# Optimization experiments

Hardware: AMD Instinct MI355X
Metric: run time of the kernel (lower is better)

Reference implementation:

```python
import jax, jax.numpy as jnp
import numpy as np

VARIANCE = (0.1, 0.2)   # SSD variance from init_kwargs
TOP_K = 1000            # max detections / NMS candidates per (image, class)


def _pairwise_iou(b):
    # b: [K,4] in point form (x1,y1,x2,y2)
    area = jnp.maximum(b[:, 2] - b[:, 0], 0.0) * jnp.maximum(b[:, 3] - b[:, 1], 0.0)
    lt = jnp.maximum(b[:, None, :2], b[None, :, :2])
    rb = jnp.minimum(b[:, None, 2:], b[None, :, 2:])
    wh = jnp.maximum(rb - lt, 0.0)
    inter = wh[..., 0] * wh[..., 1]
    union = area[:, None] + area[None, :] - inter
    return inter / jnp.maximum(union, 1e-12)


def _nms_pack(points, csboxes, scores, conf_thresh, nms_thresh):
    # points/csboxes: [P,4]; scores: [P]. Returns [TOP_K, 5] = (score, cx, cy, w, h)
    K = TOP_K
    masked = jnp.where(scores >= conf_thresh, scores, -jnp.inf)
    vals, idx = jax.lax.top_k(masked, K)          # sorted descending
    p = points[idx]                                # [K,4] point form
    cs = csboxes[idx]                              # [K,4] center-size form
    valid = vals >= conf_thresh
    iou = _pairwise_iou(p)                         # [K,K]
    ar = jnp.arange(K)

    def body(i, keep):
        # box i (if kept) suppresses all lower-scored boxes with IoU > thresh
        sup = (iou[i] > nms_thresh) & (ar > i) & keep[i]
        return keep & ~sup

    keep = jax.lax.fori_loop(0, K, body, valid)
    rows = jnp.concatenate([vals[:, None], cs], axis=1)        # [K,5]
    pos = jnp.where(keep, jnp.cumsum(keep) - 1, K)             # compact kept rows to front
    out = jnp.zeros((K, 5), rows.dtype).at[pos].set(rows, mode='drop')
    return out


def setup_inputs() -> dict:
    key = jax.random.key(0)
    k1, k2, k3, k4 = jax.random.split(key, 4)
    B, P, C = 8, 120000, 5
    loc_data = jax.random.normal(k1, (B, 4, P), dtype=jnp.float32) * 0.5
    conf_data = jax.random.normal(k2, (B, C, P), dtype=jnp.float32)
    cxcy = jax.random.uniform(k3, (P, 2), dtype=jnp.float32)
    wh = 0.01 + 0.29 * jax.random.uniform(k4, (P, 2), dtype=jnp.float32)
    prior_data = jnp.concatenate([cxcy, wh], axis=1)           # (cx,cy,w,h) in [0,1]
    return {
        'loc_data': loc_data,
        'conf_data': conf_data,
        'prior_data': prior_data,
        'conf_thresh': jnp.float32(0.05),
        'nms_thresh': jnp.float32(0.5),
    }


def reference(loc_data, conf_data, prior_data, conf_thresh, nms_thresh):
    v0, v1 = VARIANCE
    # softmax over class dim, drop background class 0 -> [B, Cfg, P]
    conf = jax.nn.softmax(conf_data, axis=1)[:, 1:]
    loc = jnp.transpose(loc_data, (0, 2, 1))                   # [B,P,4]
    # SSD decode -> center-size boxes
    cxcy = prior_data[None, :, :2] + loc[..., :2] * v0 * prior_data[None, :, 2:]
    wh = prior_data[None, :, 2:] * jnp.exp(loc[..., 2:] * v1)
    cs = jnp.concatenate([cxcy, wh], axis=-1)                  # [B,P,4] center-size
    pts = jnp.concatenate([cxcy - wh / 2, cxcy + wh / 2], axis=-1)  # [B,P,4] point form
    per_class = jax.vmap(_nms_pack, in_axes=(None, None, 0, None, None))
    per_image = jax.vmap(per_class, in_axes=(0, 0, 0, None, None))
    return per_image(pts, cs, conf, conf_thresh, nms_thresh)   # [B, Cfg, TOP_K, 5]
```

## Files before the change

kernel.cpp:

```cpp
#include <hip/hip_runtime.h>
#include <cstdint>
#include <cstddef>

typedef unsigned long long ull;

#define KTOP   1000
#define CAP    4096
#define HBITS  14
#define HB     (1 << HBITS)
#define HSHIFT (32 - HBITS)
#define ROWS   1024
#define WORDS  16
#define HCHUNK 16

__global__ void decode_kernel(const float* __restrict__ loc,
                              const float* __restrict__ conf,
                              const float* __restrict__ prior,
                              float* __restrict__ scores,
                              float* __restrict__ cs,
                              unsigned* __restrict__ histz,
                              int histW,
                              int B, int C, int P) {
#pragma clang fp contract(off)
    int t = blockIdx.x * blockDim.x + threadIdx.x;

    for (int i = t; i < histW; i += gridDim.x * blockDim.x) histz[i] = 0u;

    if (t >= B * P) return;
    int b = t / P;
    int p = t - b * P;

    float x[8];
    float m = -INFINITY;
    for (int c = 0; c < C; ++c) {
        x[c] = conf[((size_t)b * C + c) * P + p];
        m = fmaxf(m, x[c]);
    }
    float sum = 0.f;
    for (int c = 0; c < C; ++c) {
        x[c] = expf(x[c] - m);
        sum += x[c];
    }
    for (int c = 1; c < C; ++c) {
        float v = x[c] / sum;
        int bc = b * (C - 1) + (c - 1);
        scores[(size_t)bc * P + p] = v;
    }

    float l0 = loc[((size_t)b * 4 + 0) * P + p];
    float l1 = loc[((size_t)b * 4 + 1) * P + p];
    float l2 = loc[((size_t)b * 4 + 2) * P + p];
    float l3 = loc[((size_t)b * 4 + 3) * P + p];
    float4 pr4 = *(const float4*)(prior + (size_t)p * 4);

    float cx = pr4.x + (l0 * 0.1f) * pr4.z;
    float cy = pr4.y + (l1 * 0.1f) * pr4.w;
    float w  = pr4.z * expf(l2 * 0.2f);
    float h  = pr4.w * expf(l3 * 0.2f);

    *(float4*)(cs + ((size_t)b * P + p) * 4) = make_float4(cx, cy, w, h);
}

__global__ void __launch_bounds__(256)
hist_kernel(const float* __restrict__ scores,
            const float* __restrict__ cthp,
            unsigned* __restrict__ hist,
            int P) {
    __shared__ unsigned sh[HB / 2];
    int bc  = blockIdx.x;
    int tid = threadIdx.x;
    float cth = *cthp;

    for (int i = tid; i < HB / 2; i += 256) sh[i] = 0u;
    __syncthreads();

    int chunk = (P + HCHUNK - 1) / HCHUNK;
    int lo = blockIdx.y * chunk;
    int hi = lo + chunk; if (hi > P) hi = P;
    const float* s = scores + (size_t)bc * P;
    for (int p = lo + tid; p < hi; p += 256) {
        float v = s[p];
        if (v >= cth) {
            unsigned bin = __float_as_uint(v) >> HSHIFT;
            atomicAdd(&sh[bin >> 1], (bin & 1u) ? 65536u : 1u);
        }
    }
    __syncthreads();

    unsigned* h = hist + (size_t)bc * HB;
    for (int i = tid; i < HB / 2; i += 256) {
        unsigned v = sh[i];
        if (v & 0xFFFFu)  atomicAdd(&h[2 * i],     v & 0xFFFFu);
        if (v >> 16)      atomicAdd(&h[2 * i + 1], v >> 16);
    }
}

__global__ void __launch_bounds__(256)
pivot_kernel(const unsigned* __restrict__ hist, unsigned* __restrict__ pivot) {
    int bc  = blockIdx.x;
    int t   = threadIdx.x;
    const unsigned* h = hist + (size_t)bc * HB;
    __shared__ unsigned T[256];

    const int per = HB / 256;
    int base = t * per;
    unsigned S = 0;
    for (int i = 0; i < per; ++i) S += h[base + i];
    T[t] = S;
    __syncthreads();

    for (int d = 1; d < 256; d <<= 1) {
        unsigned add = (t + d < 256) ? T[t + d] : 0u;
        __syncthreads();
        T[t] += add;
        __syncthreads();
    }

    unsigned Tt = T[t];
    unsigned Tn = (t + 1 < 256) ? T[t + 1] : 0u;
    if (Tt >= (unsigned)KTOP && Tn < (unsigned)KTOP) {
        unsigned cum = Tn;
        for (int i = per - 1; i >= 0; --i) {
            cum += h[base + i];
            if (cum >= (unsigned)KTOP) { pivot[bc] = (unsigned)(base + i); break; }
        }
    }
    if (t == 0 && T[0] < (unsigned)KTOP) pivot[bc] = 0u;
}

__global__ void __launch_bounds__(256)
gather_kernel(const float* __restrict__ scores,
              const unsigned* __restrict__ pivot,
              unsigned* __restrict__ cnt,
              ull* __restrict__ cand,
              const float* __restrict__ cthp, int P) {
    __shared__ unsigned wsum[4];
    __shared__ unsigned s_base;
    int bc = blockIdx.x;
    const float* s = scores + (size_t)bc * P;
    float cth = *cthp;
    unsigned pv = pivot[bc];
    int nchunk = gridDim.y;
    int chunk = (P + nchunk - 1) / nchunk;
    int lo = blockIdx.y * chunk;
    int hi = lo + chunk; if (hi > P) hi = P;
    int tid  = threadIdx.x;
    int lane = tid & 63;
    int wid  = tid >> 6;

    unsigned mycnt = 0;
    for (int p = lo + tid; p < hi; p += 256) {
        float v = s[p];
        unsigned k = __float_as_uint(v);
        if (v >= cth && (k >> HSHIFT) >= pv) ++mycnt;
    }
    unsigned x = mycnt;
    for (int d = 1; d < 64; d <<= 1) {
        unsigned y = (unsigned)__shfl_up((int)x, d);
        if (lane >= d) x += y;
    }
    if (lane == 63) wsum[wid] = x;
    __syncthreads();
    if (tid == 0) {
        unsigned tot = 0;
        for (int w = 0; w < 4; ++w) { unsigned t2 = wsum[w]; wsum[w] = tot; tot += t2; }
        s_base = tot ? atomicAdd(&cnt[bc], tot) : 0u;
    }
    __syncthreads();
    unsigned off = s_base + wsum[wid] + (x - mycnt);

    ull* cb = cand + (size_t)bc * CAP;
    for (int p = lo + tid; p < hi; p += 256) {
        float v = s[p];
        unsigned k = __float_as_uint(v);
        if (v >= cth && (k >> HSHIFT) >= pv) {
            if (off < CAP)
                cb[off] = ((ull)k << 32) | (unsigned)(~(unsigned)p);
            ++off;
        }
    }
}

__global__ void __launch_bounds__(1024)
sort_kernel(const ull* __restrict__ cand,
            const unsigned* __restrict__ cnt,
            const float* __restrict__ cs,
            float* __restrict__ rows,
            float4* __restrict__ pbox,
            float* __restrict__ bar,
            int* __restrict__ nselArr,
            int P, int Cfg) {
#pragma clang fp contract(off)
    int bc  = blockIdx.x;
    int b   = bc / Cfg;
    int tid = threadIdx.x;
    __shared__ ull sbuf[CAP];

    int M = (int)cnt[bc]; if (M > CAP) M = CAP;
    int nsel = M < KTOP ? M : KTOP;
    if (tid == 0) nselArr[bc] = nsel;

    int n = 1024;
    while (n < M) n <<= 1;
    for (int i = tid; i < n; i += 1024)
        sbuf[i] = (i < M) ? cand[(size_t)bc * CAP + i] : 0ull;
    __syncthreads();

    for (unsigned k = 2; k <= (unsigned)n; k <<= 1) {
        for (unsigned j = k >> 1; j > 0; j >>= 1) {
            for (unsigned i = tid; i < (unsigned)n; i += 1024) {
                unsigned ixj = i ^ j;
                if (ixj > i) {
                    bool up = ((i & k) == 0u);
                    ull a = sbuf[i], bb = sbuf[ixj];
                    if ((a > bb) == up) { sbuf[i] = bb; sbuf[ixj] = a; }
                }
            }
            __syncthreads();
        }
    }

    for (int r = tid; r < nsel; r += 1024) {
        ull e = sbuf[n - 1 - r];
        float sc = __uint_as_float((unsigned)(e >> 32));
        int idx = (int)(~(unsigned)e);
        const float* c4 = cs + ((size_t)b * P + idx) * 4;
        float cx = c4[0], cy = c4[1], w = c4[2], h = c4[3];
        float x1 = cx - w / 2.f, y1 = cy - h / 2.f;
        float x2 = cx + w / 2.f, y2 = cy + h / 2.f;
        size_t sb = (size_t)bc * ROWS + r;
        pbox[sb] = make_float4(x1, y1, x2, y2);
        bar[sb]  = fmaxf(x2 - x1, 0.f) * fmaxf(y2 - y1, 0.f);
        float* rr = rows + ((size_t)bc * KTOP + r) * 5;
        rr[0] = sc; rr[1] = cx; rr[2] = cy; rr[3] = w; rr[4] = h;
    }
}

__global__ void __launch_bounds__(1024)
mask_kernel(const float4* __restrict__ pbox,
            const float* __restrict__ bar,
            const int* __restrict__ nselArr,
            const float* __restrict__ nthp,
            ull* __restrict__ mask) {
#pragma clang fp contract(off)
    int bc   = blockIdx.x;
    int tile = blockIdx.y;
    int tid  = threadIdx.x;
    int nsel = nselArr[bc];
    float nth = *nthp;

    __shared__ float4 sbox[ROWS];
    __shared__ float  sar[ROWS];
    size_t sb = (size_t)bc * ROWS;
    sbox[tid] = pbox[sb + tid];
    sar[tid]  = bar[sb + tid];
    __syncthreads();

    int wv   = tid >> 6;
    int lane = tid & 63;
    int i0   = tile * 64 + (wv << 2);

    float4 bi[4]; float ai[4];
    #pragma unroll
    for (int r = 0; r < 4; ++r) { bi[r] = sbox[i0 + r]; ai[r] = sar[i0 + r]; }

    ull rowbits[4] = {0ull, 0ull, 0ull, 0ull};
    for (int w = 0; w < WORDS; ++w) {
        int j = (w << 6) + lane;
        float4 bj = sbox[j];
        float  aj = sar[j];
        #pragma unroll
        for (int r = 0; r < 4; ++r) {
            int i = i0 + r;
            float ww = fmaxf(fminf(bi[r].z, bj.z) - fmaxf(bi[r].x, bj.x), 0.f);
            float hh = fmaxf(fminf(bi[r].w, bj.w) - fmaxf(bi[r].y, bj.y), 0.f);
            float inter = ww * hh;
            float uni = ai[r] + aj - inter;
            float iou = inter / fmaxf(uni, 1e-12f);
            bool ok = (j > i) && (j < nsel) && (iou > nth);
            ull bits = __ballot(ok);
            if (lane == w) rowbits[r] = bits;
        }
    }
    #pragma unroll
    for (int r = 0; r < 4; ++r)
        if (lane < WORDS)
            mask[(((size_t)bc * ROWS + (i0 + r)) << 4) + lane] = rowbits[r];
}

__device__ __forceinline__ void nms_chunk_body(
    int c, int nchunk, int lane, int g, int w,
    const ull* __restrict__ mrow, ull* sm,
    ull (&pr)[16], ull (&st)[16], ull& S)
{
    int cb = (c & 1) << 10;
    int nb = ((c + 1) & 1) << 10;
    if (c + 2 < nchunk) {
        #pragma unroll
        for (int k = 0; k < 16; ++k)
            pr[k] = mrow[(size_t)(c + 2) * 1024 + k * 64 + lane];
    }

    ull cur = __shfl(S, c);
    ull dbuf[16], dnxt[16];
    #pragma unroll
    for (int k = 0; k < 16; ++k) dbuf[k] = sm[cb + (k << 4) + c];
    #pragma unroll
    for (int grp = 0; grp < 4; ++grp) {
        if (grp < 3) {
            #pragma unroll
            for (int k = 0; k < 16; ++k)
                dnxt[k] = sm[cb + ((((grp + 1) << 4) + k) << 4) + c];
        }
        #pragma unroll
        for (int k = 0; k < 16; ++k) {
            int i = (grp << 4) + k;
            ull supm = (ull)((long long)(cur << (63 - i)) >> 63);
            cur |= dbuf[k] & ~supm;
        }
        if (grp < 3) {
            #pragma unroll
            for (int k = 0; k < 16; ++k) dbuf[k] = dnxt[k];
        }
    }
    ull kbits = ~cur;

    unsigned sub = (unsigned)((kbits >> (g << 4)) & 0xFFFFull);
    int rbase2 = cb + (g << 8) + w;
    ull part = 0ull;
    #pragma unroll
    for (int i = 0; i < 16; ++i) {
        ull v = sm[rbase2 + (i << 4)];
        part |= v & (ull)(0ll - (long long)((sub >> i) & 1u));
    }
    part |= __shfl_xor(part, 16);
    part |= __shfl_xor(part, 32);
    S |= part;
    if (lane == c) S = cur;

    if (c + 1 < nchunk) {
        #pragma unroll
        for (int k = 0; k < 16; ++k) sm[nb + k * 64 + lane] = st[k];
    }
}

__global__ void __launch_bounds__(256)
reduce_pack_kernel(const ull* __restrict__ mask,
                   const int* __restrict__ nselArr,
                   const float* __restrict__ rows,
                   float* __restrict__ out) {
    int bc  = blockIdx.x;
    int tid = threadIdx.x;
    int nsel = nselArr[bc];
    const ull* mrow = mask + ((size_t)bc * ROWS << 4);

    __shared__ ull sm[2048];
    __shared__ ull kw[WORDS];
    __shared__ unsigned pref[WORDS + 1];

    if (tid < 64) {
        int lane = tid;
        int nchunk = (nsel + 63) >> 6;
        ull S = 0ull;
        int g = lane >> 4;
        int w = lane & 15;

        ull ra[16], rb[16];
        if (nchunk > 0) {
            #pragma unroll
            for (int k = 0; k < 16; ++k) ra[k] = mrow[k * 64 + lane];
            if (nchunk > 1) {
                #pragma unroll
                for (int k = 0; k < 16; ++k) rb[k] = mrow[1024 + k * 64 + lane];
            }
            #pragma unroll
            for (int k = 0; k < 16; ++k) sm[k * 64 + lane] = ra[k];

            #pragma unroll 1
            for (int cc = 0; cc < 8; ++cc) {
                int c0 = cc << 1;
                if (c0 >= nchunk) break;
                nms_chunk_body(c0, nchunk, lane, g, w, mrow, sm, ra, rb, S);
                int c1 = c0 + 1;
                if (c1 >= nchunk) break;
                nms_chunk_body(c1, nchunk, lane, g, w, mrow, sm, rb, ra, S);
            }
        }

        if (lane < WORDS) {
            int base_i = lane << 6;
            ull valid = 0ull;
            int rem = nsel - base_i;
            if (rem > 0) valid = (rem >= 64) ? ~0ull : ((1ull << rem) - 1ull);
            kw[lane] = (~S) & valid;
        }
    }
    __syncthreads();

    if (tid == 0) {
        unsigned c = 0;
        for (int w = 0; w < WORDS; ++w) { pref[w] = c; c += (unsigned)__popcll(kw[w]); }
        pref[WORDS] = c;
    }
    __syncthreads();
    unsigned tot = pref[WORDS];

    const float* rbase = rows + (size_t)bc * KTOP * 5;
    float* obase = out + (size_t)bc * KTOP * 5;
    for (int r = tid; r < KTOP; r += 256) {
        ull wv = kw[r >> 6];
        if ((wv >> (r & 63)) & 1ull) {
            int pos = (int)pref[r >> 6] + __popcll(wv & ((1ull << (r & 63)) - 1ull));
            const float* rr = rbase + r * 5;
            float* oo = obase + pos * 5;
            oo[0] = rr[0]; oo[1] = rr[1]; oo[2] = rr[2]; oo[3] = rr[3]; oo[4] = rr[4];
        }
        if (r >= (int)tot) {
            float* oo = obase + r * 5;
            oo[0] = 0.f; oo[1] = 0.f; oo[2] = 0.f; oo[3] = 0.f; oo[4] = 0.f;
        }
    }
}

extern "C" void kernel_launch(void* const* d_in, const int* in_sizes, int n_in,
                              void* d_out, int out_size, void* d_ws, size_t ws_size,
                              hipStream_t stream) {
    (void)n_in; (void)out_size; (void)ws_size;
    const float* loc   = (const float*)d_in[0];
    const float* conf  = (const float*)d_in[1];
    const float* prior = (const float*)d_in[2];
    const float* cth   = (const float*)d_in[3];
    const float* nth   = (const float*)d_in[4];
    float* out = (float*)d_out;

    int P   = in_sizes[2] / 4;
    int B   = in_sizes[0] / (4 * P);
    int C   = in_sizes[1] / (B * P);
    int Cfg = C - 1;
    int NBC = B * Cfg;

    char* base = (char*)d_ws;
    size_t off = 0;
    auto carve = [&](size_t bytes) { char* p = base + off; off = (off + bytes + 255) & ~(size_t)255; return p; };

    float4*   pbox   = (float4*)  carve((size_t)NBC * ROWS * 16);
    ull*      cand   = (ull*)     carve((size_t)NBC * CAP * 8);
    ull*      mask   = (ull*)     carve((size_t)NBC * ROWS * WORDS * 8);
    float*    scores = (float*)   carve((size_t)NBC * P * 4);
    float*    cs     = (float*)   carve((size_t)B * P * 4 * 4);
    float*    rows   = (float*)   carve((size_t)NBC * KTOP * 5 * 4);
    float*    bar    = (float*)   carve((size_t)NBC * ROWS * 4);
    unsigned* hist   = (unsigned*)carve((size_t)NBC * HB * 4 + (size_t)NBC * 4);
    unsigned* cnt    = hist + (size_t)NBC * HB;
    unsigned* pivot  = (unsigned*)carve((size_t)NBC * 4);
    int*      nselA  = (int*)     carve((size_t)NBC * 4);

    int histW = NBC * HB + NBC;

    int n1 = B * P;
    decode_kernel<<<(n1 + 255) / 256, 256, 0, stream>>>(loc, conf, prior, scores, cs, hist, histW, B, C, P);
    hist_kernel<<<dim3(NBC, HCHUNK), 256, 0, stream>>>(scores, cth, hist, P);
    pivot_kernel<<<NBC, 256, 0, stream>>>(hist, pivot);
    gather_kernel<<<dim3(NBC, 32), 256, 0, stream>>>(scores, pivot, cnt, cand, cth, P);
    sort_kernel<<<NBC, 1024, 0, stream>>>(cand, cnt, cs, rows, pbox, bar, nselA, P, Cfg);
    mask_kernel<<<dim3(NBC, ROWS / 64), 1024, 0, stream>>>(pbox, bar, nselA, nth, mask);
    reduce_pack_kernel<<<NBC, 256, 0, stream>>>(mask, nselA, rows, out);
}
```

Measured before the change: 210.6 us.

## Defer box decode to selected candidates, fuse pivot into hist, single-pass gather

Drops full box decoding from the decode kernel and decodes only the selected top candidates inside the sort kernel. The pivot kernel is folded into the histogram kernel using a last-block-done atomic counter. Gather becomes single-pass, staging through LDS with ballot compaction. Sort adds a secondary histogram pre-filter so it sorts about 1024 entries instead of up to 4096, and the mask kernel skips tiles and words below the diagonal or beyond nsel. Together these cut global memory traffic, kernel launches and sort work, at the cost of added atomics and more complex code.

```diff
diff --git a/kernel.cpp b/kernel.cpp
--- a/kernel.cpp
+++ b/kernel.cpp
@@ -12,12 +12,10 @@
 #define ROWS   1024
 #define WORDS  16
 #define HCHUNK 16
-
-__global__ void decode_kernel(const float* __restrict__ loc,
-                              const float* __restrict__ conf,
-                              const float* __restrict__ prior,
+#define GSTAGE 4096
+
+__global__ void decode_kernel(const float* __restrict__ conf,
                               float* __restrict__ scores,
-                              float* __restrict__ cs,
                               unsigned* __restrict__ histz,
                               int histW,
                               int B, int C, int P) {
@@ -46,27 +44,18 @@
         int bc = b * (C - 1) + (c - 1);
         scores[(size_t)bc * P + p] = v;
     }
-
-    float l0 = loc[((size_t)b * 4 + 0) * P + p];
-    float l1 = loc[((size_t)b * 4 + 1) * P + p];
-    float l2 = loc[((size_t)b * 4 + 2) * P + p];
-    float l3 = loc[((size_t)b * 4 + 3) * P + p];
-    float4 pr4 = *(const float4*)(prior + (size_t)p * 4);
-
-    float cx = pr4.x + (l0 * 0.1f) * pr4.z;
-    float cy = pr4.y + (l1 * 0.1f) * pr4.w;
-    float w  = pr4.z * expf(l2 * 0.2f);
-    float h  = pr4.w * expf(l3 * 0.2f);
-
-    *(float4*)(cs + ((size_t)b * P + p) * 4) = make_float4(cx, cy, w, h);
 }
 
 __global__ void __launch_bounds__(256)
 hist_kernel(const float* __restrict__ scores,
             const float* __restrict__ cthp,
             unsigned* __restrict__ hist,
+            unsigned* __restrict__ done,
+            unsigned* __restrict__ pivot,
             int P) {
     __shared__ unsigned sh[HB / 2];
+    __shared__ unsigned T[256];
+    __shared__ unsigned s_tk;
     int bc  = blockIdx.x;
     int tid = threadIdx.x;
     float cth = *cthp;
@@ -93,39 +82,40 @@
         if (v & 0xFFFFu)  atomicAdd(&h[2 * i],     v & 0xFFFFu);
         if (v >> 16)      atomicAdd(&h[2 * i + 1], v >> 16);
     }
-}
-
-__global__ void __launch_bounds__(256)
-pivot_kernel(const unsigned* __restrict__ hist, unsigned* __restrict__ pivot) {
-    int bc  = blockIdx.x;
-    int t   = threadIdx.x;
-    const unsigned* h = hist + (size_t)bc * HB;
-    __shared__ unsigned T[256];
+    __syncthreads();
+
+    if (tid == 0) {
+        __threadfence();
+        s_tk = __hip_atomic_fetch_add(&done[bc], 1u, __ATOMIC_ACQ_REL, __HIP_MEMORY_SCOPE_AGENT);
+    }
+    __syncthreads();
+    if (s_tk != (unsigned)(gridDim.y - 1)) return;
 
     const int per = HB / 256;
-    int base = t * per;
+    int base = tid * per;
     unsigned S = 0;
-    for (int i = 0; i < per; ++i) S += h[base + i];
-    T[t] = S;
+    for (int i = 0; i < per; ++i)
+        S += __hip_atomic_load(&h[base + i], __ATOMIC_RELAXED, __HIP_MEMORY_SCOPE_AGENT);
+    T[tid] = S;
     __syncthreads();
 
     for (int d = 1; d < 256; d <<= 1) {
-        unsigned add = (t + d < 256) ? T[t + d] : 0u;
-        __syncthreads();
-        T[t] += add;
-        __syncthreads();
-    }
-
-    unsigned Tt = T[t];
-    unsigned Tn = (t + 1 < 256) ? T[t + 1] : 0u;
+        unsigned add = (tid + d < 256) ? T[tid + d] : 0u;
+        __syncthreads();
+        T[tid] += add;
+        __syncthreads();
+    }
+
+    unsigned Tt = T[tid];
+    unsigned Tn = (tid + 1 < 256) ? T[tid + 1] : 0u;
     if (Tt >= (unsigned)KTOP && Tn < (unsigned)KTOP) {
         unsigned cum = Tn;
         for (int i = per - 1; i >= 0; --i) {
-            cum += h[base + i];
+            cum += __hip_atomic_load(&h[base + i], __ATOMIC_RELAXED, __HIP_MEMORY_SCOPE_AGENT);
             if (cum >= (unsigned)KTOP) { pivot[bc] = (unsigned)(base + i); break; }
         }
     }
-    if (t == 0 && T[0] < (unsigned)KTOP) pivot[bc] = 0u;
+    if (tid == 0 && T[0] < (unsigned)KTOP) pivot[bc] = 0u;
 }
 
 __global__ void __launch_bounds__(256)
@@ -134,7 +124,8 @@
               unsigned* __restrict__ cnt,
               ull* __restrict__ cand,
               const float* __restrict__ cthp, int P) {
-    __shared__ unsigned wsum[4];
+    __shared__ ull stage[GSTAGE];
+    __shared__ unsigned l_cnt;
     __shared__ unsigned s_base;
     int bc = blockIdx.x;
     const float* s = scores + (size_t)bc * P;
@@ -146,45 +137,48 @@
     int hi = lo + chunk; if (hi > P) hi = P;
     int tid  = threadIdx.x;
     int lane = tid & 63;
-    int wid  = tid >> 6;
-
-    unsigned mycnt = 0;
-    for (int p = lo + tid; p < hi; p += 256) {
-        float v = s[p];
-        unsigned k = __float_as_uint(v);
-        if (v >= cth && (k >> HSHIFT) >= pv) ++mycnt;
-    }
-    unsigned x = mycnt;
-    for (int d = 1; d < 64; d <<= 1) {
-        unsigned y = (unsigned)__shfl_up((int)x, d);
-        if (lane >= d) x += y;
-    }
-    if (lane == 63) wsum[wid] = x;
-    __syncthreads();
-    if (tid == 0) {
-        unsigned tot = 0;
-        for (int w = 0; w < 4; ++w) { unsigned t2 = wsum[w]; wsum[w] = tot; tot += t2; }
-        s_base = tot ? atomicAdd(&cnt[bc], tot) : 0u;
-    }
-    __syncthreads();
-    unsigned off = s_base + wsum[wid] + (x - mycnt);
-
+
+    if (tid == 0) l_cnt = 0u;
+    __syncthreads();
+
+    for (int p0 = lo; p0 < hi; p0 += 256) {
+        int p = p0 + tid;
+        bool q = false; unsigned k = 0u;
+        if (p < hi) {
+            float v = s[p];
+            k = __float_as_uint(v);
+            q = (v >= cth) && ((k >> HSHIFT) >= pv);
+        }
+        ull mb = __ballot(q);
+        if (mb) {
+            unsigned wbase = 0u;
+            if (lane == 0) wbase = atomicAdd(&l_cnt, (unsigned)__popcll(mb));
+            wbase = (unsigned)__shfl((int)wbase, 0);
+            if (q) {
+                unsigned pos = wbase + (unsigned)__popcll(mb & ((1ull << lane) - 1ull));
+                stage[pos] = ((ull)k << 32) | (unsigned)(~(unsigned)p);
+            }
+        }
+    }
+    __syncthreads();
+
+    unsigned tot = l_cnt;
+    if (tid == 0) s_base = tot ? atomicAdd(&cnt[bc], tot) : 0u;
+    __syncthreads();
+    unsigned base = s_base;
     ull* cb = cand + (size_t)bc * CAP;
-    for (int p = lo + tid; p < hi; p += 256) {
-        float v = s[p];
-        unsigned k = __float_as_uint(v);
-        if (v >= cth && (k >> HSHIFT) >= pv) {
-            if (off < CAP)
-                cb[off] = ((ull)k << 32) | (unsigned)(~(unsigned)p);
-            ++off;
-        }
+    for (unsigned i = tid; i < tot; i += 256) {
+        unsigned off = base + i;
+        if (off < CAP) cb[off] = stage[i];
     }
 }
 
 __global__ void __launch_bounds__(1024)
 sort_kernel(const ull* __restrict__ cand,
             const unsigned* __restrict__ cnt,
-            const float* __restrict__ cs,
+            const unsigned* __restrict__ pivot,
+            const float* __restrict__ loc,
+            const float* __restrict__ prior,
             float* __restrict__ rows,
             float4* __restrict__ pbox,
             float* __restrict__ bar,
@@ -195,15 +189,61 @@
     int b   = bc / Cfg;
     int tid = threadIdx.x;
     __shared__ ull sbuf[CAP];
+    __shared__ unsigned h2[1024];
+    __shared__ unsigned s_hi, s_spv, s_m2, s_pos;
 
     int M = (int)cnt[bc]; if (M > CAP) M = CAP;
     int nsel = M < KTOP ? M : KTOP;
     if (tid == 0) nselArr[bc] = nsel;
 
+    for (int i = tid; i < M; i += 1024)
+        sbuf[i] = cand[(size_t)bc * CAP + i];
+    __syncthreads();
+
+    int Meff = M;
+    if (M > 1024) {
+        unsigned pv = pivot[bc];
+        h2[tid] = 0u;
+        if (tid == 0) { s_hi = 0u; s_pos = 0u; s_spv = 0u; s_m2 = (unsigned)M; }
+        __syncthreads();
+        for (int i = tid; i < M; i += 1024) {
+            unsigned sb32 = (unsigned)(sbuf[i] >> 32);
+            if ((sb32 >> HSHIFT) > pv) atomicAdd(&s_hi, 1u);
+            else atomicAdd(&h2[(sb32 >> 8) & 1023u], 1u);
+        }
+        __syncthreads();
+        unsigned hicnt = s_hi;
+        for (int d = 1; d < 1024; d <<= 1) {
+            unsigned add = (tid + d < 1024) ? h2[tid + d] : 0u;
+            __syncthreads();
+            h2[tid] += add;
+            __syncthreads();
+        }
+        unsigned A  = hicnt + h2[tid];
+        unsigned Bv = hicnt + ((tid + 1 < 1024) ? h2[tid + 1] : 0u);
+        if (A >= (unsigned)KTOP && Bv < (unsigned)KTOP) { s_spv = (unsigned)tid; s_m2 = A; }
+        __syncthreads();
+        unsigned thr24 = ((unsigned)pv << 10) | s_spv;
+        Meff = (int)s_m2;
+        ull my[4];
+        #pragma unroll
+        for (int j = 0; j < 4; ++j) { int i = tid + (j << 10); my[j] = (i < M) ? sbuf[i] : 0ull; }
+        __syncthreads();
+        #pragma unroll
+        for (int j = 0; j < 4; ++j) {
+            int i = tid + (j << 10);
+            if (i < M && (unsigned)(my[j] >> 40) >= thr24) {
+                unsigned pos = atomicAdd(&s_pos, 1u);
+                sbuf[pos] = my[j];
+            }
+        }
+        __syncthreads();
+    }
+
     int n = 1024;
-    while (n < M) n <<= 1;
+    while (n < Meff) n <<= 1;
     for (int i = tid; i < n; i += 1024)
-        sbuf[i] = (i < M) ? cand[(size_t)bc * CAP + i] : 0ull;
+        if (i >= Meff) sbuf[i] = 0ull;
     __syncthreads();
 
     for (unsigned k = 2; k <= (unsigned)n; k <<= 1) {
@@ -224,8 +264,15 @@
         ull e = sbuf[n - 1 - r];
         float sc = __uint_as_float((unsigned)(e >> 32));
         int idx = (int)(~(unsigned)e);
-        const float* c4 = cs + ((size_t)b * P + idx) * 4;
-        float cx = c4[0], cy = c4[1], w = c4[2], h = c4[3];
+        float l0 = loc[((size_t)b * 4 + 0) * P + idx];
+        float l1 = loc[((size_t)b * 4 + 1) * P + idx];
+        float l2 = loc[((size_t)b * 4 + 2) * P + idx];
+        float l3 = loc[((size_t)b * 4 + 3) * P + idx];
+        float4 pr4 = *(const float4*)(prior + (size_t)idx * 4);
+        float cx = pr4.x + (l0 * 0.1f) * pr4.z;
+        float cy = pr4.y + (l1 * 0.1f) * pr4.w;
+        float w  = pr4.z * expf(l2 * 0.2f);
+        float h  = pr4.w * expf(l3 * 0.2f);
         float x1 = cx - w / 2.f, y1 = cy - h / 2.f;
         float x2 = cx + w / 2.f, y2 = cy + h / 2.f;
         size_t sb = (size_t)bc * ROWS + r;
@@ -260,26 +307,29 @@
     int lane = tid & 63;
     int i0   = tile * 64 + (wv << 2);
 
-    float4 bi[4]; float ai[4];
-    #pragma unroll
-    for (int r = 0; r < 4; ++r) { bi[r] = sbox[i0 + r]; ai[r] = sar[i0 + r]; }
-
     ull rowbits[4] = {0ull, 0ull, 0ull, 0ull};
-    for (int w = 0; w < WORDS; ++w) {
-        int j = (w << 6) + lane;
-        float4 bj = sbox[j];
-        float  aj = sar[j];
+    if (i0 < nsel) {
+        float4 bi[4]; float ai[4];
         #pragma unroll
-        for (int r = 0; r < 4; ++r) {
-            int i = i0 + r;
-            float ww = fmaxf(fminf(bi[r].z, bj.z) - fmaxf(bi[r].x, bj.x), 0.f);
-            float hh = fmaxf(fminf(bi[r].w, bj.w) - fmaxf(bi[r].y, bj.y), 0.f);
-            float inter = ww * hh;
-            float uni = ai[r] + aj - inter;
-            float iou = inter / fmaxf(uni, 1e-12f);
-            bool ok = (j > i) && (j < nsel) && (iou > nth);
-            ull bits = __ballot(ok);
-            if (lane == w) rowbits[r] = bits;
+        for (int r = 0; r < 4; ++r) { bi[r] = sbox[i0 + r]; ai[r] = sar[i0 + r]; }
+
+        int whi = (nsel + 63) >> 6; if (whi > WORDS) whi = WORDS;
+        for (int w = tile; w < whi; ++w) {
+            int j = (w << 6) + lane;
+            float4 bj = sbox[j];
+            float  aj = sar[j];
+            #pragma unroll
+            for (int r = 0; r < 4; ++r) {
+                int i = i0 + r;
+                float ww = fmaxf(fminf(bi[r].z, bj.z) - fmaxf(bi[r].x, bj.x), 0.f);
+                float hh = fmaxf(fminf(bi[r].w, bj.w) - fmaxf(bi[r].y, bj.y), 0.f);
+                float inter = ww * hh;
+                float uni = ai[r] + aj - inter;
+                float iou = inter / fmaxf(uni, 1e-12f);
+                bool ok = (j > i) && (j < nsel) && (iou > nth);
+                ull bits = __ballot(ok);
+                if (lane == w) rowbits[r] = bits;
+            }
         }
     }
     #pragma unroll
@@ -447,22 +497,24 @@
     ull*      cand   = (ull*)     carve((size_t)NBC * CAP * 8);
     ull*      mask   = (ull*)     carve((size_t)NBC * ROWS * WORDS * 8);
     float*    scores = (float*)   carve((size_t)NBC * P * 4);
-    float*    cs     = (float*)   carve((size_t)B * P * 4 * 4);
     float*    rows   = (float*)   carve((size_t)NBC * KTOP * 5 * 4);
     float*    bar    = (float*)   carve((size_t)NBC * ROWS * 4);
-    unsigned* hist   = (unsigned*)carve((size_t)NBC * HB * 4 + (size_t)NBC * 4);
+    unsigned* hist   = (unsigned*)carve((size_t)NBC * HB * 4 + (size_t)2 * NBC * 4);
     unsigned* cnt    = hist + (size_t)NBC * HB;
+    unsigned* done   = cnt + NBC;
     unsigned* pivot  = (unsigned*)carve((size_t)NBC * 4);
     int*      nselA  = (int*)     carve((size_t)NBC * 4);
 
-    int histW = NBC * HB + NBC;
+    int histW = NBC * HB + 2 * NBC;
+
+    int GY = (P + GSTAGE - 1) / GSTAGE;
+    if (GY < 32) GY = 32;
 
     int n1 = B * P;
-    decode_kernel<<<(n1 + 255) / 256, 256, 0, stream>>>(loc, conf, prior, scores, cs, hist, histW, B, C, P);
-    hist_kernel<<<dim3(NBC, HCHUNK), 256, 0, stream>>>(scores, cth, hist, P);
-    pivot_kernel<<<NBC, 256, 0, stream>>>(hist, pivot);
-    gather_kernel<<<dim3(NBC, 32), 256, 0, stream>>>(scores, pivot, cnt, cand, cth, P);
-    sort_kernel<<<NBC, 1024, 0, stream>>>(cand, cnt, cs, rows, pbox, bar, nselA, P, Cfg);
+    decode_kernel<<<(n1 + 255) / 256, 256, 0, stream>>>(conf, scores, hist, histW, B, C, P);
+    hist_kernel<<<dim3(NBC, HCHUNK), 256, 0, stream>>>(scores, cth, hist, done, pivot, P);
+    gather_kernel<<<dim3(NBC, GY), 256, 0, stream>>>(scores, pivot, cnt, cand, cth, P);
+    sort_kernel<<<NBC, 1024, 0, stream>>>(cand, cnt, pivot, loc, prior, rows, pbox, bar, nselA, P, Cfg);
     mask_kernel<<<dim3(NBC, ROWS / 64), 1024, 0, stream>>>(pbox, bar, nselA, nth, mask);
     reduce_pack_kernel<<<NBC, 256, 0, stream>>>(mask, nselA, rows, out);
 }
```

Result: slower. 220.8 us (+4.9%).
